# Kernel tuning notes

Measured on AMD Instinct MI355X. Metric: run time of the kernel, lower is better.

## Reference

```python
import jax, jax.numpy as jnp
import numpy as np

N_NODES = 50000
N_EDGES = 800000
IN_CH = 128
OUT_CH = 64
HEADS = 4
NEG_SLOPE = 0.2


def setup_inputs() -> dict:
    key = jax.random.key(0)
    k1, k2, k3, k4, k5 = jax.random.split(key, 5)
    x = jax.random.normal(k1, (N_NODES, IN_CH), dtype=jnp.float32)
    edge_index = jax.random.randint(k2, (2, N_EDGES), 0, N_NODES, dtype=jnp.int64)
    # Glorot-ish scaled params
    W = jax.random.normal(k3, (IN_CH, HEADS * OUT_CH), dtype=jnp.float32) * (1.0 / np.sqrt(IN_CH))
    att_src = jax.random.normal(k4, (HEADS, OUT_CH), dtype=jnp.float32) * (1.0 / np.sqrt(OUT_CH))
    att_dst = jax.random.normal(k5, (HEADS, OUT_CH), dtype=jnp.float32) * (1.0 / np.sqrt(OUT_CH))
    bias = jnp.zeros((HEADS * OUT_CH,), dtype=jnp.float32)
    return {"x": x, "edge_index": edge_index, "W": W, "att_src": att_src, "att_dst": att_dst, "bias": bias}


def reference(x, edge_index, W, att_src, att_dst, bias):
    N = x.shape[0]
    H, C = att_src.shape
    # PyG GATConv default add_self_loops=True
    loops = jnp.arange(N, dtype=edge_index.dtype)
    src = jnp.concatenate([edge_index[0], loops])  # message source j
    dst = jnp.concatenate([edge_index[1], loops])  # message target i
    # Linear transform per head: [N, H, C]
    h = (x @ W).reshape(N, H, C)
    # Per-node attention logits: [N, H]
    a_src = jnp.sum(h * att_src[None], axis=-1)
    a_dst = jnp.sum(h * att_dst[None], axis=-1)
    # Per-edge raw score (alpha_src from source node, alpha_dst from target node)
    e = jax.nn.leaky_relu(a_src[src] + a_dst[dst], NEG_SLOPE)  # [E, H]
    # Segment-softmax over incoming edges of each target node
    m = jax.ops.segment_max(e, dst, num_segments=N)  # [N, H]
    m = jnp.where(jnp.isfinite(m), m, 0.0)  # nodes with no edges -> 0
    ex = jnp.exp(e - m[dst])
    denom = jax.ops.segment_sum(ex, dst, num_segments=N)  # [N, H]
    alpha = ex / (denom[dst] + 1e-16)  # [E, H]
    # Weighted aggregate of source features: [N, H, C]
    msg = h[src] * alpha[:, :, None]
    out = jax.ops.segment_sum(msg, dst, num_segments=N)
    # concat=True: flatten heads, add bias
    return out.reshape(N, H * C) + bias
```

## Files before the change

### kernel.cpp

```cpp
#include <hip/hip_runtime.h>

#define N_NODES 50000
#define N_EDGES 800000
#define IN_CH 128
#define OUT_CH 64
#define HEADS 4
#define HC 256
#define NEG_SLOPE 0.2f
#define GEMM_BLOCKS 782
#define COUNT_BLOCKS 782
#define SCAN_BLOCKS 49

#define HB_OFF       0UL
#define WSW_OFF      25600000UL
#define ASRC_OFF     25665536UL
#define ADST_OFF     26465536UL
#define COUNTS_OFF   27265536UL
#define OFFSETS_OFF  27465536UL
#define BSUMS_OFF    27665536UL
#define RANK_OFF     27666560UL
#define REC_OFF      30866560UL

typedef __attribute__((ext_vector_type(8))) __fp16 f16x8;
typedef __attribute__((ext_vector_type(4))) unsigned uint32x4;
typedef __attribute__((ext_vector_type(4))) float f32x4;
typedef __attribute__((ext_vector_type(2))) __fp16 fp16x2;

__device__ __forceinline__ unsigned f2h2(float a, float b) {
  fp16x2 h = __builtin_amdgcn_cvt_pkrtz(a, b);
  return __builtin_bit_cast(unsigned, h);
}
__device__ __forceinline__ void fma2(float& a0, float& a1, unsigned u, float e) {
  fp16x2 h = __builtin_bit_cast(fp16x2, u);
  a0 = fmaf((float)h.x, e, a0);
  a1 = fmaf((float)h.y, e, a1);
}
__device__ __forceinline__ float lrelu(float e) {
  return e > 0.f ? e : NEG_SLOPE * e;
}
__device__ __forceinline__ float exhalf(uint4 r, int hd) {
  unsigned pair = (hd & 2) ? r.z : r.y;
  fp16x2 h = __builtin_bit_cast(fp16x2, pair);
  return (hd & 1) ? (float)h.y : (float)h.x;
}

__global__ __launch_bounds__(256) void init_k(const float* __restrict__ W,
                                              unsigned short* __restrict__ Wsw,
                                              int* __restrict__ counts) {
  if (blockIdx.x < 16) {
    int idx = blockIdx.x * 256 + threadIdx.x;
    int l = idx & 63;
    int kc = (idx >> 6) & 3;
    int t = idx >> 8;
    int kbase = kc * 32 + (l >> 4) * 8;
    int col = t * 16 + (l & 15);
    unsigned int p[4];
#pragma unroll
    for (int j = 0; j < 4; ++j) {
      p[j] = f2h2(W[(size_t)(kbase + 2 * j) * HC + col],
                  W[(size_t)(kbase + 2 * j + 1) * HC + col]);
    }
    *(uint4*)(Wsw + (size_t)idx * 8) = make_uint4(p[0], p[1], p[2], p[3]);
  } else {
    int i = (blockIdx.x - 16) * 256 + threadIdx.x;
    if (i < N_NODES) counts[i] = 0;
  }
}

__global__ __launch_bounds__(256) void gemm_count(const float* __restrict__ x,
                                                  const unsigned short* __restrict__ Wsw,
                                                  const float* __restrict__ att_s,
                                                  const float* __restrict__ att_d,
                                                  const int* __restrict__ dstv,
                                                  unsigned short* __restrict__ hb,
                                                  float* __restrict__ a_src,
                                                  float* __restrict__ a_dst,
                                                  int* __restrict__ counts,
                                                  int* __restrict__ rank) {
  __shared__ float Cs[4][16][128];

  if (blockIdx.x >= GEMM_BLOCKS) {
    int base = (blockIdx.x - GEMM_BLOCKS) * 1024 + threadIdx.x;
#pragma unroll
    for (int k = 0; k < 4; ++k) {
      int e = base + k * 256;
      if (e < N_EDGES) rank[e] = atomicAdd(&counts[dstv[e]], 1);
    }
    return;
  }

  const int wave = threadIdx.x >> 6;
  const int l = threadIdx.x & 63;
  const int q = l >> 4;
  const int m = l & 15;
  const int mrow = blockIdx.x * 64 + wave * 16 + m;
  const bool mvalid = mrow < N_NODES;
  const int rc = mvalid ? mrow : (N_NODES - 1);

  f16x8 a[4];
  const float* xr = x + (size_t)rc * IN_CH + q * 8;
#pragma unroll
  for (int kc = 0; kc < 4; ++kc) {
    float4 u = *(const float4*)(xr + kc * 32);
    float4 v = *(const float4*)(xr + kc * 32 + 4);
    uint32x4 t;
    t[0] = f2h2(u.x, u.y);
    t[1] = f2h2(u.z, u.w);
    t[2] = f2h2(v.x, v.y);
    t[3] = f2h2(v.z, v.w);
    a[kc] = __builtin_bit_cast(f16x8, t);
  }

  float as = 0.f, ad = 0.f;
  unsigned short* hrow = hb + (size_t)mrow * HC + q * 64;
  const int sw = m << 2;

#pragma unroll
  for (int P = 0; P < 2; ++P) {
    if (P) __syncthreads();
#pragma unroll
    for (int tt = 0; tt < 8; ++tt) {
      int t = ((tt >> 1) << 2) + P * 2 + (tt & 1);
      f32x4 acc = {0.f, 0.f, 0.f, 0.f};
#pragma unroll
      for (int kc = 0; kc < 4; ++kc) {
        f16x8 b = *(const f16x8*)(Wsw + ((size_t)(t * 4 + kc) * 64 + l) * 8);
        acc = __builtin_amdgcn_mfma_f32_16x16x32_f16(a[kc], b, acc, 0, 0, 0);
      }
#pragma unroll
      for (int r = 0; r < 4; ++r) {
        int row = q * 4 + r;
        Cs[wave][row][(tt * 16 + m) ^ (row << 2)] = acc[r];
      }
    }
    __syncthreads();

#pragma unroll
    for (int i = 0; i < 4; ++i) {
      int lcol = q * 32 + i * 8;
      float4 c1 = *(const float4*)&Cs[wave][m][(lcol) ^ sw];
      float4 c2 = *(const float4*)&Cs[wave][m][(lcol + 4) ^ sw];
      int ch = q * 64 + P * 32 + i * 8;
      float4 s1 = *(const float4*)(att_s + ch);
      float4 s2 = *(const float4*)(att_s + ch + 4);
      float4 d1 = *(const float4*)(att_d + ch);
      float4 d2 = *(const float4*)(att_d + ch + 4);
      as += c1.x * s1.x + c1.y * s1.y + c1.z * s1.z + c1.w * s1.w;
      as += c2.x * s2.x + c2.y * s2.y + c2.z * s2.z + c2.w * s2.w;
      ad += c1.x * d1.x + c1.y * d1.y + c1.z * d1.z + c1.w * d1.w;
      ad += c2.x * d2.x + c2.y * d2.y + c2.z * d2.z + c2.w * d2.w;
      if (mvalid) {
        uint4 p;
        p.x = f2h2(c1.x, c1.y);
        p.y = f2h2(c1.z, c1.w);
        p.z = f2h2(c2.x, c2.y);
        p.w = f2h2(c2.z, c2.w);
        *(uint4*)(hrow + P * 32 + i * 8) = p;
      }
    }
  }
  if (mvalid) {
    a_src[mrow * HEADS + q] = as;
    a_dst[mrow * HEADS + q] = ad;
  }
}

__global__ __launch_bounds__(256) void scan1(const int* __restrict__ counts,
                                             int* __restrict__ offsets,
                                             int* __restrict__ bsums) {
  __shared__ int sd[256];
  const int base = blockIdx.x * 1024;
  const int t = threadIdx.x;
  int v[4];
  int tsum = 0;
#pragma unroll
  for (int k = 0; k < 4; ++k) {
    int i = base + t * 4 + k;
    v[k] = (i < N_NODES) ? counts[i] : 0;
    tsum += v[k];
  }
  sd[t] = tsum;
  __syncthreads();
  for (int off = 1; off < 256; off <<= 1) {
    int xval = (t >= off) ? sd[t - off] : 0;
    __syncthreads();
    sd[t] += xval;
    __syncthreads();
  }
  int excl = sd[t] - tsum;
  int run = excl;
#pragma unroll
  for (int k = 0; k < 4; ++k) {
    int i = base + t * 4 + k;
    if (i < N_NODES) offsets[i] = run;
    run += v[k];
  }
  if (t == 255) bsums[blockIdx.x] = sd[255];
}

__global__ __launch_bounds__(256) void scan23(int* __restrict__ offsets,
                                              const int* __restrict__ bsums) {
  __shared__ int s_add;
  if (threadIdx.x < 64) {
    int lane = threadIdx.x;
    int v = (lane < SCAN_BLOCKS) ? bsums[lane] : 0;
#pragma unroll
    for (int o = 1; o < 64; o <<= 1) {
      int t = __shfl_up(v, o);
      if (lane >= o) v += t;
    }
    int b = blockIdx.x;
    int pre = (b == 0) ? 0 : __shfl(v, b - 1);
    if (lane == 0) s_add = pre;
  }
  __syncthreads();
  const int add = s_add;
  const int base = blockIdx.x * 1024;
  const int t = threadIdx.x;
#pragma unroll
  for (int k = 0; k < 4; ++k) {
    int i = base + t * 4 + k;
    if (i < N_NODES) offsets[i] += add;
  }
}

__global__ __launch_bounds__(256) void scatter_k(const int* __restrict__ src,
                                                 const int* __restrict__ dst,
                                                 const int* __restrict__ rank,
                                                 const int* __restrict__ offsets,
                                                 const float* __restrict__ a_src,
                                                 const float* __restrict__ a_dst,
                                                 uint4* __restrict__ rec) {
  int e = blockIdx.x * 256 + threadIdx.x;
  if (e < N_EDGES) {
    int s = src[e];
    int d = dst[e];
    float4 as = *(const float4*)(a_src + s * 4);
    float4 ad = *(const float4*)(a_dst + d * 4);
    float ex0 = __expf(lrelu(as.x + ad.x));
    float ex1 = __expf(lrelu(as.y + ad.y));
    float ex2 = __expf(lrelu(as.z + ad.z));
    float ex3 = __expf(lrelu(as.w + ad.w));
    int pos = offsets[d] + rank[e];
    rec[pos] = make_uint4((unsigned)s, f2h2(ex0, ex1), f2h2(ex2, ex3), 0u);
  }
}

__global__ __launch_bounds__(256) void aggregate(const unsigned short* __restrict__ hb,
                                                 const float* __restrict__ a_src,
                                                 const float* __restrict__ a_dst,
                                                 const int* __restrict__ counts,
                                                 const int* __restrict__ offsets,
                                                 const uint4* __restrict__ rec,
                                                 const float* __restrict__ bias,
                                                 float* __restrict__ out) {
  const int node = blockIdx.x * 4 + (threadIdx.x >> 6);
  const int l = threadIdx.x & 63;
  const int g = l >> 4;
  const int q = l & 15;
  const int hd = q >> 2;
  const int cb = q * 32;
  const int deg = counts[node];
  const int start = offsets[node];
  const char* hbase = (const char*)hb;

  float denom = 0.f;
  float acc[16];
#pragma unroll
  for (int k = 0; k < 16; ++k) acc[k] = 0.f;

  for (int j = 0; j + g < deg; j += 8) {
    int i0 = start + j + g;
    bool v1 = (j + g + 4) < deg;
    int i1 = v1 ? (i0 + 4) : i0;
    uint4 r0 = rec[i0];
    uint4 r1 = rec[i1];
    int s0 = (int)r0.x;
    int s1 = (int)r1.x;
    float ex0 = exhalf(r0, hd);
    float ex1 = v1 ? exhalf(r1, hd) : 0.f;
    const char* hp0 = hbase + (size_t)s0 * 512 + cb;
    const char* hp1 = hbase + (size_t)s1 * 512 + cb;
    uint4 A0 = *(const uint4*)hp0;
    uint4 A1 = *(const uint4*)(hp0 + 16);
    uint4 B0 = *(const uint4*)hp1;
    uint4 B1 = *(const uint4*)(hp1 + 16);
    denom += ex0 + ex1;
    fma2(acc[0],  acc[1],  A0.x, ex0);  fma2(acc[2],  acc[3],  A0.y, ex0);
    fma2(acc[4],  acc[5],  A0.z, ex0);  fma2(acc[6],  acc[7],  A0.w, ex0);
    fma2(acc[8],  acc[9],  A1.x, ex0);  fma2(acc[10], acc[11], A1.y, ex0);
    fma2(acc[12], acc[13], A1.z, ex0);  fma2(acc[14], acc[15], A1.w, ex0);
    fma2(acc[0],  acc[1],  B0.x, ex1);  fma2(acc[2],  acc[3],  B0.y, ex1);
    fma2(acc[4],  acc[5],  B0.z, ex1);  fma2(acc[6],  acc[7],  B0.w, ex1);
    fma2(acc[8],  acc[9],  B1.x, ex1);  fma2(acc[10], acc[11], B1.y, ex1);
    fma2(acc[12], acc[13], B1.z, ex1);  fma2(acc[14], acc[15], B1.w, ex1);
  }

  denom += __shfl_xor(denom, 16);
  denom += __shfl_xor(denom, 32);
#pragma unroll
  for (int k = 0; k < 16; ++k) {
    acc[k] += __shfl_xor(acc[k], 16);
    acc[k] += __shfl_xor(acc[k], 32);
  }

  float es = a_src[node * HEADS + hd] + a_dst[node * HEADS + hd];
  float exs = __expf(lrelu(es));
  denom += exs;
  const char* hp = hbase + (size_t)node * 512 + cb;
  uint4 h0 = *(const uint4*)hp;
  uint4 h1 = *(const uint4*)(hp + 16);
  fma2(acc[0],  acc[1],  h0.x, exs);  fma2(acc[2],  acc[3],  h0.y, exs);
  fma2(acc[4],  acc[5],  h0.z, exs);  fma2(acc[6],  acc[7],  h0.w, exs);
  fma2(acc[8],  acc[9],  h1.x, exs);  fma2(acc[10], acc[11], h1.y, exs);
  fma2(acc[12], acc[13], h1.z, exs);  fma2(acc[14], acc[15], h1.w, exs);

  float inv = 1.f / (denom + 1e-16f);
  int c = q * 16 + g * 4;
  float4 bv = *(const float4*)(bias + c);
  float4 o = make_float4(acc[g * 4 + 0] * inv + bv.x, acc[g * 4 + 1] * inv + bv.y,
                         acc[g * 4 + 2] * inv + bv.z, acc[g * 4 + 3] * inv + bv.w);
  *(float4*)(out + (size_t)node * HC + c) = o;
}

extern "C" void kernel_launch(void* const* d_in, const int* in_sizes, int n_in,
                              void* d_out, int out_size, void* d_ws, size_t ws_size,
                              hipStream_t stream) {
  const float* x     = (const float*)d_in[0];
  const int*   ei    = (const int*)d_in[1];
  const float* W     = (const float*)d_in[2];
  const float* att_s = (const float*)d_in[3];
  const float* att_d = (const float*)d_in[4];
  const float* bias  = (const float*)d_in[5];
  float* out = (float*)d_out;

  char* ws = (char*)d_ws;
  unsigned short* hb  = (unsigned short*)(ws + HB_OFF);
  unsigned short* Wsw = (unsigned short*)(ws + WSW_OFF);
  float* a_src  = (float*)(ws + ASRC_OFF);
  float* a_dst  = (float*)(ws + ADST_OFF);
  int* counts   = (int*)(ws + COUNTS_OFF);
  int* offsets  = (int*)(ws + OFFSETS_OFF);
  int* bsums    = (int*)(ws + BSUMS_OFF);
  int* rank     = (int*)(ws + RANK_OFF);
  uint4* rec    = (uint4*)(ws + REC_OFF);

  const int* src = ei;
  const int* dst = ei + N_EDGES;

  init_k<<<16 + 196, 256, 0, stream>>>(W, Wsw, counts);
  gemm_count<<<GEMM_BLOCKS + COUNT_BLOCKS, 256, 0, stream>>>(
      x, Wsw, att_s, att_d, dst, hb, a_src, a_dst, counts, rank);
  scan1<<<SCAN_BLOCKS, 256, 0, stream>>>(counts, offsets, bsums);
  scan23<<<SCAN_BLOCKS, 256, 0, stream>>>(offsets, bsums);
  scatter_k<<<3125, 256, 0, stream>>>(src, dst, rank, offsets, a_src, a_dst, rec);
  aggregate<<<12500, 256, 0, stream>>>(hb, a_src, a_dst, counts, offsets, rec, bias, out);
}
```

Before: 224.8 us.

## Swap MFMA operands to compute transposed tiles and drop LDS staging

```diff
diff --git a/kernel.cpp b/kernel.cpp
--- a/kernel.cpp
+++ b/kernel.cpp
@@ -77,8 +77,6 @@
                                                   float* __restrict__ a_dst,
                                                   int* __restrict__ counts,
                                                   int* __restrict__ rank) {
-  __shared__ float Cs[4][16][128];
-
   if (blockIdx.x >= GEMM_BLOCKS) {
     int base = (blockIdx.x - GEMM_BLOCKS) * 1024 + threadIdx.x;
 #pragma unroll
@@ -111,57 +109,42 @@
     a[kc] = __builtin_bit_cast(f16x8, t);
   }
 
-  float as = 0.f, ad = 0.f;
-  unsigned short* hrow = hb + (size_t)mrow * HC + q * 64;
-  const int sw = m << 2;
-
-#pragma unroll
-  for (int P = 0; P < 2; ++P) {
-    if (P) __syncthreads();
-#pragma unroll
-    for (int tt = 0; tt < 8; ++tt) {
-      int t = ((tt >> 1) << 2) + P * 2 + (tt & 1);
-      f32x4 acc = {0.f, 0.f, 0.f, 0.f};
-#pragma unroll
-      for (int kc = 0; kc < 4; ++kc) {
-        f16x8 b = *(const f16x8*)(Wsw + ((size_t)(t * 4 + kc) * 64 + l) * 8);
-        acc = __builtin_amdgcn_mfma_f32_16x16x32_f16(a[kc], b, acc, 0, 0, 0);
-      }
-#pragma unroll
-      for (int r = 0; r < 4; ++r) {
-        int row = q * 4 + r;
-        Cs[wave][row][(tt * 16 + m) ^ (row << 2)] = acc[r];
-      }
-    }
-    __syncthreads();
-
-#pragma unroll
-    for (int i = 0; i < 4; ++i) {
-      int lcol = q * 32 + i * 8;
-      float4 c1 = *(const float4*)&Cs[wave][m][(lcol) ^ sw];
-      float4 c2 = *(const float4*)&Cs[wave][m][(lcol + 4) ^ sw];
-      int ch = q * 64 + P * 32 + i * 8;
-      float4 s1 = *(const float4*)(att_s + ch);
-      float4 s2 = *(const float4*)(att_s + ch + 4);
-      float4 d1 = *(const float4*)(att_d + ch);
-      float4 d2 = *(const float4*)(att_d + ch + 4);
-      as += c1.x * s1.x + c1.y * s1.y + c1.z * s1.z + c1.w * s1.w;
-      as += c2.x * s2.x + c2.y * s2.y + c2.z * s2.z + c2.w * s2.w;
-      ad += c1.x * d1.x + c1.y * d1.y + c1.z * d1.z + c1.w * d1.w;
-      ad += c2.x * d2.x + c2.y * d2.y + c2.z * d2.z + c2.w * d2.w;
-      if (mvalid) {
-        uint4 p;
-        p.x = f2h2(c1.x, c1.y);
-        p.y = f2h2(c1.z, c1.w);
-        p.z = f2h2(c2.x, c2.y);
-        p.w = f2h2(c2.z, c2.w);
-        *(uint4*)(hrow + P * 32 + i * 8) = p;
-      }
-    }
-  }
-  if (mvalid) {
-    a_src[mrow * HEADS + q] = as;
-    a_dst[mrow * HEADS + q] = ad;
+  float as[4] = {0.f, 0.f, 0.f, 0.f};
+  float ad[4] = {0.f, 0.f, 0.f, 0.f};
+  unsigned short* hrow = hb + (size_t)mrow * HC;
+
+#pragma unroll
+  for (int t = 0; t < 16; ++t) {
+    f32x4 acc = {0.f, 0.f, 0.f, 0.f};
+#pragma unroll
+    for (int kc = 0; kc < 4; ++kc) {
+      f16x8 w = *(const f16x8*)(Wsw + ((size_t)(t * 4 + kc) * 64 + l) * 8);
+      acc = __builtin_amdgcn_mfma_f32_16x16x32_f16(w, a[kc], acc, 0, 0, 0);
+    }
+    const int ch = t * 16 + q * 4;
+    const int hh = t >> 2;
+    float4 sv = *(const float4*)(att_s + ch);
+    float4 dv = *(const float4*)(att_d + ch);
+    as[hh] += acc[0] * sv.x + acc[1] * sv.y + acc[2] * sv.z + acc[3] * sv.w;
+    ad[hh] += acc[0] * dv.x + acc[1] * dv.y + acc[2] * dv.z + acc[3] * dv.w;
+    if (mvalid) {
+      uint2 p;
+      p.x = f2h2(acc[0], acc[1]);
+      p.y = f2h2(acc[2], acc[3]);
+      *(uint2*)(hrow + ch) = p;
+    }
+  }
+
+#pragma unroll
+  for (int h = 0; h < 4; ++h) {
+    as[h] += __shfl_xor(as[h], 16);
+    as[h] += __shfl_xor(as[h], 32);
+    ad[h] += __shfl_xor(ad[h], 16);
+    ad[h] += __shfl_xor(ad[h], 32);
+  }
+  if (l < 16 && mvalid) {
+    *(float4*)(a_src + (size_t)mrow * 4) = make_float4(as[0], as[1], as[2], as[3]);
+    *(float4*)(a_dst + (size_t)mrow * 4) = make_float4(ad[0], ad[1], ad[2], ad[3]);
   }
 }
 
```

New measurement: 224.2 us. Within noise of the previous version (-0.3%).
